# Kernel optimization log

Measured on AMD Instinct MI355X. Metric: run time of the kernel, lower is better.

Reference implementation:

```python
import jax, jax.numpy as jnp
import numpy as np

NEG = -1.0e9

def setup_inputs() -> dict:
    key = jax.random.key(0)
    k1, k2 = jax.random.split(key)
    B, S, D = 4, 4096, 256
    encodings = jax.random.normal(k1, (B, S, D), dtype=jnp.float32)
    # nn.Linear weight [out, in]; Linear applies x @ W.T
    W = jax.random.normal(k2, (D, D), dtype=jnp.float32) * (1.0 / np.sqrt(D))
    return {"encodings": encodings, "W": W}

def reference(encodings, W):
    B, S, D = encodings.shape
    enc_mult_W = jnp.einsum('bsd,ed->bse', encodings, W)          # Linear, no bias
    sims = jnp.einsum('bqd,bkd->bqk', encodings, enc_mult_W)       # E @ (EW^T)^T
    scaled = sims / jnp.asarray(np.sqrt(D), dtype=sims.dtype)
    # causal mask: positions k > q masked out (top-left softmax == 1)
    mask = jnp.triu(jnp.ones((S, S), dtype=bool), k=1)
    scaled = jnp.where(mask[None, :, :], jnp.asarray(NEG, scaled.dtype), scaled)
    attn = jax.nn.softmax(scaled, axis=-1)
    return jnp.einsum('bqk,bkd->bqd', attn, encodings)
```

## Files before the change

### kernel.cpp

```cpp
#include <hip/hip_runtime.h>
#include <hip/hip_bf16.h>
#include <cstdint>
#include <cstddef>

typedef __attribute__((ext_vector_type(4))) float f32x4;
typedef __attribute__((ext_vector_type(8))) short s16x8;
typedef __attribute__((ext_vector_type(4))) unsigned int u32x4;

#define SDIM 4096
#define DDIM 256

#define GLOAD_LDS16(g, s)                                                      \
  __builtin_amdgcn_global_load_lds(                                            \
      (const __attribute__((address_space(1))) void*)(g),                      \
      (__attribute__((address_space(3))) void*)(s), 16, 0, 0)

__device__ __forceinline__ unsigned short cvt_bf16(float f) {
  union { float f; unsigned int u; } v;
  v.f = f;
  unsigned int u = v.u;
  unsigned int r = (u + 0x7FFFu + ((u >> 16) & 1u)) >> 16;
  return (unsigned short)r;
}

__device__ __forceinline__ float bf2f(unsigned short s) {
  union { unsigned int u; float f; } v;
  v.u = ((unsigned int)s) << 16;
  return v.f;
}

__global__ __launch_bounds__(256) void k_convw(const float* __restrict__ W,
                                               unsigned short* __restrict__ Wb) {
  int i = (blockIdx.x * 256 + threadIdx.x) * 8;
  f32x4 a = *(const f32x4*)(W + i);
  f32x4 b = *(const f32x4*)(W + i + 4);
  s16x8 o;
#pragma unroll
  for (int j = 0; j < 4; ++j) {
    o[j] = (short)cvt_bf16(a[j]);
    o[4 + j] = (short)cvt_bf16(b[j]);
  }
  *(s16x8*)(Wb + i) = o;
}

__global__ __launch_bounds__(256) void k_projv(const float* __restrict__ E,
                                               const unsigned short* __restrict__ Wb,
                                               unsigned short* __restrict__ Kp,
                                               unsigned short* __restrict__ Vt) {
  __shared__ unsigned short tile[64][264];
  const int tid = threadIdx.x;
  const int w = tid >> 6, l = tid & 63, lhi = l >> 4, llo = l & 15;
  const int m0g = blockIdx.x * 64;
  const int m0 = m0g + w * 16;
  f32x4 acc[16];
#pragma unroll
  for (int n = 0; n < 16; ++n) acc[n] = (f32x4){0.f, 0.f, 0.f, 0.f};
  const float* arow = E + (size_t)(m0 + llo) * DDIM;
#pragma unroll
  for (int kd = 0; kd < 8; ++kd) {
    const int dbase = kd * 32 + lhi * 8;
    f32x4 a0 = *(const f32x4*)(arow + dbase);
    f32x4 a1 = *(const f32x4*)(arow + dbase + 4);
    s16x8 af;
#pragma unroll
    for (int j = 0; j < 4; ++j) {
      af[j] = (short)cvt_bf16(a0[j]);
      af[4 + j] = (short)cvt_bf16(a1[j]);
    }
    *(s16x8*)(&tile[w * 16 + llo][dbase]) = af;
#pragma unroll
    for (int n = 0; n < 16; ++n) {
      s16x8 bf = *(const s16x8*)(Wb + (n * 16 + llo) * DDIM + dbase);
      acc[n] = __builtin_amdgcn_mfma_f32_16x16x32_bf16(af, bf, acc[n], 0, 0, 0);
    }
  }
  __syncthreads();
  {
    const int d = tid;
    const int b = m0g >> 12, s0 = m0g & 4095;
    unsigned short* vo = Vt + ((size_t)(b * DDIM) + d) * SDIM + s0;
#pragma unroll
    for (int g = 0; g < 8; ++g) {
      s16x8 pk;
#pragma unroll
      for (int j = 0; j < 8; ++j) pk[j] = (short)tile[g * 8 + j][d];
      *(s16x8*)(vo + g * 8) = pk;
    }
  }
  const float sc = 1.4426950408889634f / 16.0f;
#pragma unroll
  for (int n = 0; n < 16; ++n) {
#pragma unroll
    for (int r = 0; r < 4; ++r) {
      Kp[(size_t)(m0 + lhi * 4 + r) * DDIM + n * 16 + llo] = cvt_bf16(acc[n][r] * sc);
    }
  }
}

__global__ __launch_bounds__(256, 2) void k_attn(const float* __restrict__ E,
                                                 const unsigned short* __restrict__ Kp,
                                                 const unsigned short* __restrict__ Vt,
                                                 unsigned short* __restrict__ Po,
                                                 float* __restrict__ Lp, int nch) {
  __shared__ u32x4 smem4[4736];
  char* smem = (char*)smem4;
  const int tid = threadIdx.x;
  const int l = tid & 63, w = tid >> 6, lhi = l >> 4, llo = l & 15;
  const int u = blockIdx.x % (4 * nch);
  const int t_ = blockIdx.x / (4 * nch);
  const int qt = 31 - t_;
  const int b = u & 3, ch = u >> 2;
  const int q0 = qt * 128;
  const int chb = ch * 4 + b;
  const int ntile = 4 * (qt + 1);
  if (ntile <= ch) return;
  const int nst = (ntile - ch + nch - 1) / nch;
  const int wq0 = q0 + w * 32;

  s16x8 qf[2][8];
#pragma unroll
  for (int s = 0; s < 2; ++s) {
    const float* Eq = E + ((size_t)(b * SDIM) + wq0 + s * 16 + llo) * DDIM;
#pragma unroll
    for (int kd = 0; kd < 8; ++kd) {
      f32x4 a0 = *(const f32x4*)(Eq + kd * 32 + lhi * 8);
      f32x4 a1 = *(const f32x4*)(Eq + kd * 32 + lhi * 8 + 4);
#pragma unroll
      for (int j = 0; j < 4; ++j) {
        qf[s][kd][j] = (short)cvt_bf16(a0[j]);
        qf[s][kd][4 + j] = (short)cvt_bf16(a1[j]);
      }
    }
  }

  f32x4 oT[2][16];
#pragma unroll
  for (int s = 0; s < 2; ++s)
#pragma unroll
    for (int n = 0; n < 16; ++n) oT[s][n] = (f32x4){0.f, 0.f, 0.f, 0.f};
  float lsum[2] = {0.f, 0.f};

  const int trow = tid >> 5;
  const int kcolb = ((tid & 31) << 4) ^ ((trow & 7) << 4);
  const char* KpB = (const char*)Kp + (size_t)b * SDIM * 512;
  const char* VtB = (const char*)Vt + (size_t)b * DDIM * (SDIM * 2);
  const char* vsb = VtB + (size_t)(tid >> 2) * 8192 + (size_t)((tid & 3) * 8) * 2;

  auto stage = [&](int t) {
    const int kv0 = (ch + nch * t) * 32;
    char* kdst = smem + ((t & 1) * 16384);
    char* vdst = smem + 32768 + ((t & 1) * 16384);
    const char* ks = KpB + (size_t)(kv0 + trow) * 512 + kcolb;
    const char* vs = vsb + (size_t)kv0 * 2;
#pragma unroll
    for (int i = 0; i < 4; ++i)
      GLOAD_LDS16(ks + (size_t)i * 4096, kdst + i * 4096 + tid * 16);
#pragma unroll
    for (int i = 0; i < 4; ++i)
      GLOAD_LDS16(vs + (size_t)i * (64 * 8192), vdst + i * 4096 + tid * 16);
  };

  stage(0);
  char* sPw = smem + 65536 + w * 2560;

  for (int t = 0; t < nst; ++t) {
    const int kv0 = (ch + nch * t) * 32;
    const char* kb_ = smem + ((t & 1) * 16384);
    const char* vb_ = smem + 32768 + ((t & 1) * 16384);

    __syncthreads();
    if (t + 1 < nst) stage(t + 1);

#pragma unroll
    for (int kb = 0; kb < 2; ++kb) {
      f32x4 sa0 = (f32x4){0.f, 0.f, 0.f, 0.f};
      f32x4 sa1 = (f32x4){0.f, 0.f, 0.f, 0.f};
      const char* krow = kb_ + (kb * 16 + llo) * 512;
      __builtin_amdgcn_s_setprio(1);
#pragma unroll
      for (int kd = 0; kd < 8; ++kd) {
        s16x8 kf = *(const s16x8*)(krow + ((kd * 64 + lhi * 16) ^ ((llo & 7) << 4)));
        sa0 = __builtin_amdgcn_mfma_f32_16x16x32_bf16(kf, qf[0][kd], sa0, 0, 0, 0);
        sa1 = __builtin_amdgcn_mfma_f32_16x16x32_bf16(kf, qf[1][kd], sa1, 0, 0, 0);
      }
      __builtin_amdgcn_s_setprio(0);
      const int kvr = kv0 + kb * 16 + lhi * 4;
#pragma unroll
      for (int s = 0; s < 2; ++s) {
        const f32x4 sa = s ? sa1 : sa0;
        const int qi = wq0 + s * 16 + llo;
        float pv[4];
#pragma unroll
        for (int rr = 0; rr < 4; ++rr) {
          float v = exp2f(sa[rr] - 32.0f);
          pv[rr] = (kvr + rr > qi) ? 0.0f : v;
        }
        lsum[s] += (pv[0] + pv[1]) + (pv[2] + pv[3]);
        unsigned int w0 = __builtin_amdgcn_perm(__float_as_uint(pv[1]),
                                                __float_as_uint(pv[0]), 0x07060302u);
        unsigned int w1 = __builtin_amdgcn_perm(__float_as_uint(pv[3]),
                                                __float_as_uint(pv[2]), 0x07060302u);
        *(uint2*)(sPw + (s * 16 + llo) * 80 + kb * 32 + lhi * 8) = make_uint2(w0, w1);
      }
    }

    s16x8 pb0 = *(const s16x8*)(sPw + llo * 80 + lhi * 16);
    s16x8 pb1 = *(const s16x8*)(sPw + (16 + llo) * 80 + lhi * 16);
    __builtin_amdgcn_s_setprio(1);
#pragma unroll
    for (int n = 0; n < 16; ++n) {
      s16x8 vf = *(const s16x8*)(vb_ + (n * 16 + llo) * 64 + lhi * 16);
      oT[0][n] = __builtin_amdgcn_mfma_f32_16x16x32_bf16(vf, pb0, oT[0][n], 0, 0, 0);
      oT[1][n] = __builtin_amdgcn_mfma_f32_16x16x32_bf16(vf, pb1, oT[1][n], 0, 0, 0);
    }
    __builtin_amdgcn_s_setprio(0);
  }

#pragma unroll
  for (int s = 0; s < 2; ++s) {
    lsum[s] += __shfl_xor(lsum[s], 16);
    lsum[s] += __shfl_xor(lsum[s], 32);
  }
#pragma unroll
  for (int s = 0; s < 2; ++s) {
    const int q = wq0 + s * 16 + llo;
    unsigned short* PoW = Po + ((size_t)chb * SDIM + q) * DDIM;
#pragma unroll
    for (int n = 0; n < 16; ++n) {
      unsigned int w0 = (unsigned int)cvt_bf16(oT[s][n][0]) |
                        ((unsigned int)cvt_bf16(oT[s][n][1]) << 16);
      unsigned int w1 = (unsigned int)cvt_bf16(oT[s][n][2]) |
                        ((unsigned int)cvt_bf16(oT[s][n][3]) << 16);
      unsigned long long v64 = (unsigned long long)w0 | ((unsigned long long)w1 << 32);
      __builtin_nontemporal_store(v64, (unsigned long long*)(PoW + n * 16 + lhi * 4));
    }
    if (lhi == 0)
      __builtin_nontemporal_store(lsum[s], &Lp[(size_t)chb * SDIM + q]);
  }
}

__global__ __launch_bounds__(256) void k_merge(const unsigned short* __restrict__ Po,
                                               const float* __restrict__ Lp,
                                               float* __restrict__ out, int nch) {
  const size_t e = ((size_t)blockIdx.x * 256 + threadIdx.x) * 8;
  const size_t f = e >> 8;
  const int s = (int)(f & 4095);
  const int cnt = min(nch, 4 * (s >> 7) + 4);
  float lt = 0.f;
  for (int c = 0; c < cnt; ++c)
    lt += __builtin_nontemporal_load(&Lp[(size_t)c * 16384 + f]);
  const float inv = 1.0f / lt;
  float acc[8] = {0.f, 0.f, 0.f, 0.f, 0.f, 0.f, 0.f, 0.f};
  for (int c = 0; c < cnt; ++c) {
    s16x8 a = __builtin_nontemporal_load((const s16x8*)(Po + (size_t)c * 4194304 + e));
#pragma unroll
    for (int j = 0; j < 8; ++j) acc[j] += bf2f((unsigned short)a[j]);
  }
  f32x4 o0, o1;
#pragma unroll
  for (int j = 0; j < 4; ++j) {
    o0[j] = acc[j] * inv;
    o1[j] = acc[4 + j] * inv;
  }
  *(f32x4*)(out + e) = o0;
  *(f32x4*)(out + e + 4) = o1;
}

extern "C" void kernel_launch(void* const* d_in, const int* in_sizes, int n_in,
                              void* d_out, int out_size, void* d_ws, size_t ws_size,
                              hipStream_t stream) {
  (void)in_sizes; (void)n_in; (void)out_size;
  const float* E = (const float*)d_in[0];
  const float* W = (const float*)d_in[1];
  float* out = (float*)d_out;
  char* ws = (char*)d_ws;

  const size_t base = 16777216ull;
  auto need = [&](int c) {
    return base + (size_t)c * 8388608ull + (size_t)c * 65536ull + 262144ull;
  };
  int nch = 2;
  if (ws_size >= need(8)) nch = 8;
  else if (ws_size >= need(4)) nch = 4;

  unsigned short* Kp = (unsigned short*)(ws);
  unsigned short* Vt = (unsigned short*)(ws + 8388608);
  unsigned short* Po = (unsigned short*)(ws + base);
  size_t lp_off = base + (size_t)nch * 8388608ull;
  float* Lp = (float*)(ws + lp_off);
  unsigned short* Wb = (unsigned short*)(ws + lp_off + (size_t)nch * 65536ull);

  k_convw<<<dim3(32), dim3(256), 0, stream>>>(W, Wb);
  k_projv<<<dim3(256), dim3(256), 0, stream>>>(E, Wb, Kp, Vt);
  k_attn<<<dim3(32 * 4 * nch), dim3(256), 0, stream>>>(E, Kp, Vt, Po, Lp, nch);
  k_merge<<<dim3(2048), dim3(256), 0, stream>>>(Po, Lp, out, nch);
}
```

Measured before the change: 151.9 us.

## Fuse split-KV merge into attention kernel via last-arriver atomic counter

Removes the separate merge kernel. Each attention block now counts its finished chunk with an atomic counter per (query tile, batch), and the last block to finish sums the partial outputs and softmax denominators and writes the final fp32 output. The chunk count is fixed at 8, the workspace-size fallback is dropped, and the counters are zeroed in the weight-conversion kernel. This saves a kernel launch and lets the merge overlap with other attention work. The cost is extra fences, an atomic per block, and a serial merge tail done by one block per tile. It also assumes the workspace is large enough.

```diff
diff --git a/kernel.cpp b/kernel.cpp
--- a/kernel.cpp
+++ b/kernel.cpp
@@ -9,6 +9,7 @@
 
 #define SDIM 4096
 #define DDIM 256
+#define NCH 8
 
 #define GLOAD_LDS16(g, s)                                                      \
   __builtin_amdgcn_global_load_lds(                                            \
@@ -30,7 +31,9 @@
 }
 
 __global__ __launch_bounds__(256) void k_convw(const float* __restrict__ W,
-                                               unsigned short* __restrict__ Wb) {
+                                               unsigned short* __restrict__ Wb,
+                                               int* __restrict__ Cnt) {
+  if (blockIdx.x == 0 && threadIdx.x < 128) Cnt[threadIdx.x] = 0;
   int i = (blockIdx.x * 256 + threadIdx.x) * 8;
   f32x4 a = *(const f32x4*)(W + i);
   f32x4 b = *(const f32x4*)(W + i + 4);
@@ -101,20 +104,22 @@
                                                  const unsigned short* __restrict__ Kp,
                                                  const unsigned short* __restrict__ Vt,
                                                  unsigned short* __restrict__ Po,
-                                                 float* __restrict__ Lp, int nch) {
+                                                 float* __restrict__ Lp,
+                                                 float* __restrict__ out,
+                                                 int* __restrict__ Cnt) {
   __shared__ u32x4 smem4[4736];
   char* smem = (char*)smem4;
   const int tid = threadIdx.x;
   const int l = tid & 63, w = tid >> 6, lhi = l >> 4, llo = l & 15;
-  const int u = blockIdx.x % (4 * nch);
-  const int t_ = blockIdx.x / (4 * nch);
+  const int u = blockIdx.x % (4 * NCH);
+  const int t_ = blockIdx.x / (4 * NCH);
   const int qt = 31 - t_;
   const int b = u & 3, ch = u >> 2;
   const int q0 = qt * 128;
   const int chb = ch * 4 + b;
   const int ntile = 4 * (qt + 1);
   if (ntile <= ch) return;
-  const int nst = (ntile - ch + nch - 1) / nch;
+  const int nst = (ntile - ch + NCH - 1) / NCH;
   const int wq0 = q0 + w * 32;
 
   s16x8 qf[2][8];
@@ -147,7 +152,7 @@
   const char* vsb = VtB + (size_t)(tid >> 2) * 8192 + (size_t)((tid & 3) * 8) * 2;
 
   auto stage = [&](int t) {
-    const int kv0 = (ch + nch * t) * 32;
+    const int kv0 = (ch + NCH * t) * 32;
     char* kdst = smem + ((t & 1) * 16384);
     char* vdst = smem + 32768 + ((t & 1) * 16384);
     const char* ks = KpB + (size_t)(kv0 + trow) * 512 + kcolb;
@@ -164,7 +169,7 @@
   char* sPw = smem + 65536 + w * 2560;
 
   for (int t = 0; t < nst; ++t) {
-    const int kv0 = (ch + nch * t) * 32;
+    const int kv0 = (ch + NCH * t) * 32;
     const char* kb_ = smem + ((t & 1) * 16384);
     const char* vb_ = smem + 32768 + ((t & 1) * 16384);
 
@@ -231,67 +236,71 @@
                         ((unsigned int)cvt_bf16(oT[s][n][1]) << 16);
       unsigned int w1 = (unsigned int)cvt_bf16(oT[s][n][2]) |
                         ((unsigned int)cvt_bf16(oT[s][n][3]) << 16);
-      unsigned long long v64 = (unsigned long long)w0 | ((unsigned long long)w1 << 32);
-      __builtin_nontemporal_store(v64, (unsigned long long*)(PoW + n * 16 + lhi * 4));
-    }
-    if (lhi == 0)
-      __builtin_nontemporal_store(lsum[s], &Lp[(size_t)chb * SDIM + q]);
-  }
-}
-
-__global__ __launch_bounds__(256) void k_merge(const unsigned short* __restrict__ Po,
-                                               const float* __restrict__ Lp,
-                                               float* __restrict__ out, int nch) {
-  const size_t e = ((size_t)blockIdx.x * 256 + threadIdx.x) * 8;
-  const size_t f = e >> 8;
-  const int s = (int)(f & 4095);
-  const int cnt = min(nch, 4 * (s >> 7) + 4);
-  float lt = 0.f;
-  for (int c = 0; c < cnt; ++c)
-    lt += __builtin_nontemporal_load(&Lp[(size_t)c * 16384 + f]);
-  const float inv = 1.0f / lt;
-  float acc[8] = {0.f, 0.f, 0.f, 0.f, 0.f, 0.f, 0.f, 0.f};
-  for (int c = 0; c < cnt; ++c) {
-    s16x8 a = __builtin_nontemporal_load((const s16x8*)(Po + (size_t)c * 4194304 + e));
-#pragma unroll
-    for (int j = 0; j < 8; ++j) acc[j] += bf2f((unsigned short)a[j]);
-  }
-  f32x4 o0, o1;
-#pragma unroll
-  for (int j = 0; j < 4; ++j) {
-    o0[j] = acc[j] * inv;
-    o1[j] = acc[4 + j] * inv;
-  }
-  *(f32x4*)(out + e) = o0;
-  *(f32x4*)(out + e + 4) = o1;
+      *(uint2*)(PoW + n * 16 + lhi * 4) = make_uint2(w0, w1);
+    }
+    if (lhi == 0) Lp[(size_t)chb * SDIM + q] = lsum[s];
+  }
+
+  const int target = (ntile < NCH) ? ntile : NCH;
+  __threadfence();
+  __syncthreads();
+  int* flag = (int*)smem;
+  if (tid == 0) {
+    int old = atomicAdd(&Cnt[qt * 4 + b], 1);
+    *flag = (old == target - 1) ? 1 : 0;
+  }
+  __syncthreads();
+  if (*flag == 0) return;
+  __threadfence();
+
+  float* sInv = (float*)smem;
+  if (tid < 128) {
+    float lt = 0.f;
+    for (int c = 0; c < target; ++c)
+      lt += Lp[(size_t)(c * 4 + b) * SDIM + q0 + tid];
+    sInv[tid] = 1.0f / lt;
+  }
+  __syncthreads();
+  float* outB = out + ((size_t)(b * SDIM) + q0) * DDIM;
+#pragma unroll
+  for (int g = 0; g < 16; ++g) {
+    const int idx = g * 2048 + tid * 8;
+    const int row = idx >> 8;
+    float acc[8] = {0.f, 0.f, 0.f, 0.f, 0.f, 0.f, 0.f, 0.f};
+    for (int c = 0; c < target; ++c) {
+      s16x8 a = *(const s16x8*)(Po + ((size_t)(c * 4 + b) * SDIM + q0) * DDIM + idx);
+#pragma unroll
+      for (int j = 0; j < 8; ++j) acc[j] += bf2f((unsigned short)a[j]);
+    }
+    const float inv = sInv[row];
+    f32x4 o0, o1;
+#pragma unroll
+    for (int j = 0; j < 4; ++j) {
+      o0[j] = acc[j] * inv;
+      o1[j] = acc[4 + j] * inv;
+    }
+    *(f32x4*)(outB + idx) = o0;
+    *(f32x4*)(outB + idx + 4) = o1;
+  }
 }
 
 extern "C" void kernel_launch(void* const* d_in, const int* in_sizes, int n_in,
                               void* d_out, int out_size, void* d_ws, size_t ws_size,
                               hipStream_t stream) {
-  (void)in_sizes; (void)n_in; (void)out_size;
+  (void)in_sizes; (void)n_in; (void)out_size; (void)ws_size;
   const float* E = (const float*)d_in[0];
   const float* W = (const float*)d_in[1];
   float* out = (float*)d_out;
   char* ws = (char*)d_ws;
 
-  const size_t base = 16777216ull;
-  auto need = [&](int c) {
-    return base + (size_t)c * 8388608ull + (size_t)c * 65536ull + 262144ull;
-  };
-  int nch = 2;
-  if (ws_size >= need(8)) nch = 8;
-  else if (ws_size >= need(4)) nch = 4;
-
   unsigned short* Kp = (unsigned short*)(ws);
   unsigned short* Vt = (unsigned short*)(ws + 8388608);
-  unsigned short* Po = (unsigned short*)(ws + base);
-  size_t lp_off = base + (size_t)nch * 8388608ull;
-  float* Lp = (float*)(ws + lp_off);
-  unsigned short* Wb = (unsigned short*)(ws + lp_off + (size_t)nch * 65536ull);
-
-  k_convw<<<dim3(32), dim3(256), 0, stream>>>(W, Wb);
+  unsigned short* Po = (unsigned short*)(ws + 16777216);
+  float* Lp = (float*)(ws + 83886080);
+  unsigned short* Wb = (unsigned short*)(ws + 84410368);
+  int* Cnt = (int*)(ws + 84541440);
+
+  k_convw<<<dim3(32), dim3(256), 0, stream>>>(W, Wb, Cnt);
   k_projv<<<dim3(256), dim3(256), 0, stream>>>(E, Wb, Kp, Vt);
-  k_attn<<<dim3(32 * 4 * nch), dim3(256), 0, stream>>>(E, Kp, Vt, Po, Lp, nch);
-  k_merge<<<dim3(2048), dim3(256), 0, stream>>>(Po, Lp, out, nch);
-}
+  k_attn<<<dim3(32 * 4 * NCH), dim3(256), 0, stream>>>(E, Kp, Vt, Po, Lp, out, Cnt);
+}
```

New measurement: 346.2 us. +127.9%, slower.

## Pair causal query tiles per 512-thread block with fixed eight-way KV split

Applied to the files above, without the earlier changes.

The attention kernel now runs 256 blocks of 512 threads. Each block handles two 256-row query tiles chosen as p and 15-p, so every block does the same amount of causal work and 8 waves share each staged K/V tile. The split over the key sequence is hard-coded to 8 chunks, so the workspace size check is gone, and the merge always sums all 8 partials. Nontemporal hints on the partial stores and loads are also dropped. In exchange, occupancy drops to one large block per CU and correctness now assumes the workspace is large enough.

```diff
diff --git a/kernel.cpp b/kernel.cpp
--- a/kernel.cpp
+++ b/kernel.cpp
@@ -9,6 +9,7 @@
 
 #define SDIM 4096
 #define DDIM 256
+#define NCH 8
 
 #define GLOAD_LDS16(g, s)                                                      \
   __builtin_amdgcn_global_load_lds(                                            \
@@ -97,162 +98,160 @@
   }
 }
 
-__global__ __launch_bounds__(256, 2) void k_attn(const float* __restrict__ E,
+__global__ __launch_bounds__(512, 1) void k_attn(const float* __restrict__ E,
                                                  const unsigned short* __restrict__ Kp,
                                                  const unsigned short* __restrict__ Vt,
                                                  unsigned short* __restrict__ Po,
-                                                 float* __restrict__ Lp, int nch) {
-  __shared__ u32x4 smem4[4736];
+                                                 float* __restrict__ Lp) {
+  __shared__ u32x4 smem4[5376];
   char* smem = (char*)smem4;
   const int tid = threadIdx.x;
   const int l = tid & 63, w = tid >> 6, lhi = l >> 4, llo = l & 15;
-  const int u = blockIdx.x % (4 * nch);
-  const int t_ = blockIdx.x / (4 * nch);
-  const int qt = 31 - t_;
+  const int u = blockIdx.x & 31;
+  const int p = blockIdx.x >> 5;
   const int b = u & 3, ch = u >> 2;
-  const int q0 = qt * 128;
   const int chb = ch * 4 + b;
-  const int ntile = 4 * (qt + 1);
-  if (ntile <= ch) return;
-  const int nst = (ntile - ch + nch - 1) / nch;
-  const int wq0 = q0 + w * 32;
-
-  s16x8 qf[2][8];
-#pragma unroll
-  for (int s = 0; s < 2; ++s) {
-    const float* Eq = E + ((size_t)(b * SDIM) + wq0 + s * 16 + llo) * DDIM;
-#pragma unroll
-    for (int kd = 0; kd < 8; ++kd) {
-      f32x4 a0 = *(const f32x4*)(Eq + kd * 32 + lhi * 8);
-      f32x4 a1 = *(const f32x4*)(Eq + kd * 32 + lhi * 8 + 4);
-#pragma unroll
-      for (int j = 0; j < 4; ++j) {
-        qf[s][kd][j] = (short)cvt_bf16(a0[j]);
-        qf[s][kd][4 + j] = (short)cvt_bf16(a1[j]);
-      }
-    }
-  }
-
-  f32x4 oT[2][16];
-#pragma unroll
-  for (int s = 0; s < 2; ++s)
-#pragma unroll
-    for (int n = 0; n < 16; ++n) oT[s][n] = (f32x4){0.f, 0.f, 0.f, 0.f};
-  float lsum[2] = {0.f, 0.f};
 
   const int trow = tid >> 5;
   const int kcolb = ((tid & 31) << 4) ^ ((trow & 7) << 4);
   const char* KpB = (const char*)Kp + (size_t)b * SDIM * 512;
   const char* VtB = (const char*)Vt + (size_t)b * DDIM * (SDIM * 2);
-  const char* vsb = VtB + (size_t)(tid >> 2) * 8192 + (size_t)((tid & 3) * 8) * 2;
-
-  auto stage = [&](int t) {
-    const int kv0 = (ch + nch * t) * 32;
-    char* kdst = smem + ((t & 1) * 16384);
-    char* vdst = smem + 32768 + ((t & 1) * 16384);
-    const char* ks = KpB + (size_t)(kv0 + trow) * 512 + kcolb;
-    const char* vs = vsb + (size_t)kv0 * 2;
-#pragma unroll
-    for (int i = 0; i < 4; ++i)
-      GLOAD_LDS16(ks + (size_t)i * 4096, kdst + i * 4096 + tid * 16);
-#pragma unroll
-    for (int i = 0; i < 4; ++i)
-      GLOAD_LDS16(vs + (size_t)i * (64 * 8192), vdst + i * 4096 + tid * 16);
-  };
-
-  stage(0);
+  const char* vsb = VtB + (size_t)(tid >> 2) * 8192 + ((tid & 3) << 4);
   char* sPw = smem + 65536 + w * 2560;
 
-  for (int t = 0; t < nst; ++t) {
-    const int kv0 = (ch + nch * t) * 32;
-    const char* kb_ = smem + ((t & 1) * 16384);
-    const char* vb_ = smem + 32768 + ((t & 1) * 16384);
-
-    __syncthreads();
-    if (t + 1 < nst) stage(t + 1);
-
-#pragma unroll
-    for (int kb = 0; kb < 2; ++kb) {
-      f32x4 sa0 = (f32x4){0.f, 0.f, 0.f, 0.f};
-      f32x4 sa1 = (f32x4){0.f, 0.f, 0.f, 0.f};
-      const char* krow = kb_ + (kb * 16 + llo) * 512;
+  for (int c2 = 0; c2 < 2; ++c2) {
+    const int qt = c2 ? (15 - p) : p;
+    const int q0 = qt * 256;
+    const int nst = qt + 1;
+    const int wq0 = q0 + w * 32;
+
+    if (c2) __syncthreads();
+
+    s16x8 qf[2][8];
+#pragma unroll
+    for (int s = 0; s < 2; ++s) {
+      const float* Eq = E + ((size_t)(b * SDIM) + wq0 + s * 16 + llo) * DDIM;
+#pragma unroll
+      for (int kd = 0; kd < 8; ++kd) {
+        f32x4 a0 = *(const f32x4*)(Eq + kd * 32 + lhi * 8);
+        f32x4 a1 = *(const f32x4*)(Eq + kd * 32 + lhi * 8 + 4);
+#pragma unroll
+        for (int j = 0; j < 4; ++j) {
+          qf[s][kd][j] = (short)cvt_bf16(a0[j]);
+          qf[s][kd][4 + j] = (short)cvt_bf16(a1[j]);
+        }
+      }
+    }
+
+    f32x4 oT[2][16];
+#pragma unroll
+    for (int s = 0; s < 2; ++s)
+#pragma unroll
+      for (int n = 0; n < 16; ++n) oT[s][n] = (f32x4){0.f, 0.f, 0.f, 0.f};
+    float lsum[2] = {0.f, 0.f};
+
+    auto stage = [&](int t) {
+      const int kv0 = (ch + NCH * t) * 32;
+      char* kdst = smem + ((t & 1) * 16384);
+      char* vdst = smem + 32768 + ((t & 1) * 16384);
+      const char* ks = KpB + (size_t)(kv0 + trow) * 512 + kcolb;
+      GLOAD_LDS16(ks, kdst + tid * 16);
+      GLOAD_LDS16(ks + 16 * 512, kdst + 8192 + tid * 16);
+      const char* vs = vsb + (size_t)kv0 * 2;
+      GLOAD_LDS16(vs, vdst + tid * 16);
+      GLOAD_LDS16(vs + (size_t)128 * 8192, vdst + 8192 + tid * 16);
+    };
+
+    stage(0);
+
+    for (int t = 0; t < nst; ++t) {
+      const int kv0 = (ch + NCH * t) * 32;
+      const char* kb_ = smem + ((t & 1) * 16384);
+      const char* vb_ = smem + 32768 + ((t & 1) * 16384);
+
+      __syncthreads();
+      if (t + 1 < nst) stage(t + 1);
+
+#pragma unroll
+      for (int kb = 0; kb < 2; ++kb) {
+        f32x4 sa0 = (f32x4){0.f, 0.f, 0.f, 0.f};
+        f32x4 sa1 = (f32x4){0.f, 0.f, 0.f, 0.f};
+        const char* krow = kb_ + (kb * 16 + llo) * 512;
+        __builtin_amdgcn_s_setprio(1);
+#pragma unroll
+        for (int kd = 0; kd < 8; ++kd) {
+          s16x8 kf = *(const s16x8*)(krow + ((kd * 64 + lhi * 16) ^ ((llo & 7) << 4)));
+          sa0 = __builtin_amdgcn_mfma_f32_16x16x32_bf16(kf, qf[0][kd], sa0, 0, 0, 0);
+          sa1 = __builtin_amdgcn_mfma_f32_16x16x32_bf16(kf, qf[1][kd], sa1, 0, 0, 0);
+        }
+        __builtin_amdgcn_s_setprio(0);
+        const int kvr = kv0 + kb * 16 + lhi * 4;
+#pragma unroll
+        for (int s = 0; s < 2; ++s) {
+          const f32x4 sa = s ? sa1 : sa0;
+          const int qi = wq0 + s * 16 + llo;
+          float pv[4];
+#pragma unroll
+          for (int rr = 0; rr < 4; ++rr) {
+            float v = exp2f(sa[rr] - 32.0f);
+            pv[rr] = (kvr + rr > qi) ? 0.0f : v;
+          }
+          lsum[s] += (pv[0] + pv[1]) + (pv[2] + pv[3]);
+          unsigned int w0 = __builtin_amdgcn_perm(__float_as_uint(pv[1]),
+                                                  __float_as_uint(pv[0]), 0x07060302u);
+          unsigned int w1 = __builtin_amdgcn_perm(__float_as_uint(pv[3]),
+                                                  __float_as_uint(pv[2]), 0x07060302u);
+          *(uint2*)(sPw + (s * 16 + llo) * 80 + kb * 32 + lhi * 8) = make_uint2(w0, w1);
+        }
+      }
+
+      s16x8 pb0 = *(const s16x8*)(sPw + llo * 80 + lhi * 16);
+      s16x8 pb1 = *(const s16x8*)(sPw + (16 + llo) * 80 + lhi * 16);
       __builtin_amdgcn_s_setprio(1);
 #pragma unroll
-      for (int kd = 0; kd < 8; ++kd) {
-        s16x8 kf = *(const s16x8*)(krow + ((kd * 64 + lhi * 16) ^ ((llo & 7) << 4)));
-        sa0 = __builtin_amdgcn_mfma_f32_16x16x32_bf16(kf, qf[0][kd], sa0, 0, 0, 0);
-        sa1 = __builtin_amdgcn_mfma_f32_16x16x32_bf16(kf, qf[1][kd], sa1, 0, 0, 0);
+      for (int n = 0; n < 16; ++n) {
+        s16x8 vf = *(const s16x8*)(vb_ + (n * 16 + llo) * 64 + lhi * 16);
+        oT[0][n] = __builtin_amdgcn_mfma_f32_16x16x32_bf16(vf, pb0, oT[0][n], 0, 0, 0);
+        oT[1][n] = __builtin_amdgcn_mfma_f32_16x16x32_bf16(vf, pb1, oT[1][n], 0, 0, 0);
       }
       __builtin_amdgcn_s_setprio(0);
-      const int kvr = kv0 + kb * 16 + lhi * 4;
-#pragma unroll
-      for (int s = 0; s < 2; ++s) {
-        const f32x4 sa = s ? sa1 : sa0;
-        const int qi = wq0 + s * 16 + llo;
-        float pv[4];
-#pragma unroll
-        for (int rr = 0; rr < 4; ++rr) {
-          float v = exp2f(sa[rr] - 32.0f);
-          pv[rr] = (kvr + rr > qi) ? 0.0f : v;
-        }
-        lsum[s] += (pv[0] + pv[1]) + (pv[2] + pv[3]);
-        unsigned int w0 = __builtin_amdgcn_perm(__float_as_uint(pv[1]),
-                                                __float_as_uint(pv[0]), 0x07060302u);
-        unsigned int w1 = __builtin_amdgcn_perm(__float_as_uint(pv[3]),
-                                                __float_as_uint(pv[2]), 0x07060302u);
-        *(uint2*)(sPw + (s * 16 + llo) * 80 + kb * 32 + lhi * 8) = make_uint2(w0, w1);
-      }
-    }
-
-    s16x8 pb0 = *(const s16x8*)(sPw + llo * 80 + lhi * 16);
-    s16x8 pb1 = *(const s16x8*)(sPw + (16 + llo) * 80 + lhi * 16);
-    __builtin_amdgcn_s_setprio(1);
-#pragma unroll
-    for (int n = 0; n < 16; ++n) {
-      s16x8 vf = *(const s16x8*)(vb_ + (n * 16 + llo) * 64 + lhi * 16);
-      oT[0][n] = __builtin_amdgcn_mfma_f32_16x16x32_bf16(vf, pb0, oT[0][n], 0, 0, 0);
-      oT[1][n] = __builtin_amdgcn_mfma_f32_16x16x32_bf16(vf, pb1, oT[1][n], 0, 0, 0);
-    }
-    __builtin_amdgcn_s_setprio(0);
-  }
-
-#pragma unroll
-  for (int s = 0; s < 2; ++s) {
-    lsum[s] += __shfl_xor(lsum[s], 16);
-    lsum[s] += __shfl_xor(lsum[s], 32);
-  }
-#pragma unroll
-  for (int s = 0; s < 2; ++s) {
-    const int q = wq0 + s * 16 + llo;
-    unsigned short* PoW = Po + ((size_t)chb * SDIM + q) * DDIM;
-#pragma unroll
-    for (int n = 0; n < 16; ++n) {
-      unsigned int w0 = (unsigned int)cvt_bf16(oT[s][n][0]) |
-                        ((unsigned int)cvt_bf16(oT[s][n][1]) << 16);
-      unsigned int w1 = (unsigned int)cvt_bf16(oT[s][n][2]) |
-                        ((unsigned int)cvt_bf16(oT[s][n][3]) << 16);
-      unsigned long long v64 = (unsigned long long)w0 | ((unsigned long long)w1 << 32);
-      __builtin_nontemporal_store(v64, (unsigned long long*)(PoW + n * 16 + lhi * 4));
-    }
-    if (lhi == 0)
-      __builtin_nontemporal_store(lsum[s], &Lp[(size_t)chb * SDIM + q]);
+    }
+
+#pragma unroll
+    for (int s = 0; s < 2; ++s) {
+      lsum[s] += __shfl_xor(lsum[s], 16);
+      lsum[s] += __shfl_xor(lsum[s], 32);
+    }
+#pragma unroll
+    for (int s = 0; s < 2; ++s) {
+      const int q = wq0 + s * 16 + llo;
+      unsigned short* PoW = Po + ((size_t)chb * SDIM + q) * DDIM;
+#pragma unroll
+      for (int n = 0; n < 16; ++n) {
+        unsigned int w0 = (unsigned int)cvt_bf16(oT[s][n][0]) |
+                          ((unsigned int)cvt_bf16(oT[s][n][1]) << 16);
+        unsigned int w1 = (unsigned int)cvt_bf16(oT[s][n][2]) |
+                          ((unsigned int)cvt_bf16(oT[s][n][3]) << 16);
+        *(uint2*)(PoW + n * 16 + lhi * 4) = make_uint2(w0, w1);
+      }
+      if (lhi == 0) Lp[(size_t)chb * SDIM + q] = lsum[s];
+    }
   }
 }
 
 __global__ __launch_bounds__(256) void k_merge(const unsigned short* __restrict__ Po,
                                                const float* __restrict__ Lp,
-                                               float* __restrict__ out, int nch) {
+                                               float* __restrict__ out) {
   const size_t e = ((size_t)blockIdx.x * 256 + threadIdx.x) * 8;
   const size_t f = e >> 8;
-  const int s = (int)(f & 4095);
-  const int cnt = min(nch, 4 * (s >> 7) + 4);
   float lt = 0.f;
-  for (int c = 0; c < cnt; ++c)
-    lt += __builtin_nontemporal_load(&Lp[(size_t)c * 16384 + f]);
+#pragma unroll
+  for (int c = 0; c < NCH; ++c) lt += Lp[(size_t)c * 16384 + f];
   const float inv = 1.0f / lt;
   float acc[8] = {0.f, 0.f, 0.f, 0.f, 0.f, 0.f, 0.f, 0.f};
-  for (int c = 0; c < cnt; ++c) {
-    s16x8 a = __builtin_nontemporal_load((const s16x8*)(Po + (size_t)c * 4194304 + e));
+#pragma unroll
+  for (int c = 0; c < NCH; ++c) {
+    s16x8 a = *(const s16x8*)(Po + (size_t)c * 4194304 + e);
 #pragma unroll
     for (int j = 0; j < 8; ++j) acc[j] += bf2f((unsigned short)a[j]);
   }
@@ -269,29 +268,20 @@
 extern "C" void kernel_launch(void* const* d_in, const int* in_sizes, int n_in,
                               void* d_out, int out_size, void* d_ws, size_t ws_size,
                               hipStream_t stream) {
-  (void)in_sizes; (void)n_in; (void)out_size;
+  (void)in_sizes; (void)n_in; (void)out_size; (void)ws_size;
   const float* E = (const float*)d_in[0];
   const float* W = (const float*)d_in[1];
   float* out = (float*)d_out;
   char* ws = (char*)d_ws;
 
-  const size_t base = 16777216ull;
-  auto need = [&](int c) {
-    return base + (size_t)c * 8388608ull + (size_t)c * 65536ull + 262144ull;
-  };
-  int nch = 2;
-  if (ws_size >= need(8)) nch = 8;
-  else if (ws_size >= need(4)) nch = 4;
-
   unsigned short* Kp = (unsigned short*)(ws);
   unsigned short* Vt = (unsigned short*)(ws + 8388608);
-  unsigned short* Po = (unsigned short*)(ws + base);
-  size_t lp_off = base + (size_t)nch * 8388608ull;
-  float* Lp = (float*)(ws + lp_off);
-  unsigned short* Wb = (unsigned short*)(ws + lp_off + (size_t)nch * 65536ull);
+  unsigned short* Po = (unsigned short*)(ws + 16777216);
+  float* Lp = (float*)(ws + 83886080);
+  unsigned short* Wb = (unsigned short*)(ws + 84410368);
 
   k_convw<<<dim3(32), dim3(256), 0, stream>>>(W, Wb);
   k_projv<<<dim3(256), dim3(256), 0, stream>>>(E, Wb, Kp, Vt);
-  k_attn<<<dim3(32 * 4 * nch), dim3(256), 0, stream>>>(E, Kp, Vt, Po, Lp, nch);
-  k_merge<<<dim3(2048), dim3(256), 0, stream>>>(Po, Lp, out, nch);
-}
+  k_attn<<<dim3(256), dim3(512), 0, stream>>>(E, Kp, Vt, Po, Lp);
+  k_merge<<<dim3(2048), dim3(256), 0, stream>>>(Po, Lp, out);
+}
```

Result: faster. 130.4 us (-14.2%).
